# Performance work log

Hardware: AMD Instinct MI355X
Metric: run time of the kernel (lower is better)

Reference implementation:

```python
import jax, jax.numpy as jnp
import numpy as np


def setup_inputs() -> dict:
    key = jax.random.key(0)
    k0, k1, k2, k3 = jax.random.split(key, 4)
    N, C, H, W, s = 2, 16, 96, 96, 2
    x = jax.random.normal(k0, (N, C, H, W), dtype=jnp.float32)
    pos_mat = jax.random.uniform(k1, (1, H * s * W * s, 3), dtype=jnp.float32)
    mask = jnp.ones((1, 1, H * s, W * s), dtype=bool)
    w1 = jax.random.normal(k2, (3, 256), dtype=jnp.float32) * 0.1
    b1 = jnp.zeros((256,), dtype=jnp.float32)
    w2 = jax.random.normal(k3, (256, 9 * C * C), dtype=jnp.float32) * 0.02
    b2 = jnp.zeros((9 * C * C,), dtype=jnp.float32)
    return {"x": x, "pos_mat": pos_mat, "mask": mask, "w1": w1, "b1": b1,
            "w2": w2, "b2": b2, "r": 2, "hr0": H * s, "hr1": W * s}


def _unfold3x3(x):
    # torch F.unfold(x, kernel_size=3, padding=1) -> [N, C*9, H*W],
    # channel ordering: c slowest, then (kh, kw).
    N, C, H, W = x.shape
    xp = jnp.pad(x, ((0, 0), (0, 0), (1, 1), (1, 1)))
    patches = jnp.stack([xp[:, :, i:i + H, j:j + W]
                         for i in range(3) for j in range(3)], axis=2)  # [N,C,9,H,W]
    return patches.reshape(N, C * 9, H * W)


def reference(x, pos_mat, mask, w1, b1, w2, b2, r, hr0, hr1):
    s = int(np.ceil(r))  # scale_int
    N, C, H, W = x.shape

    # Pos2Weight hypernetwork: Linear(3,256) -> LeakyReLU(0.2) -> Linear(256, 9*C*C)
    p = pos_mat.reshape(-1, 3)                       # [H*s*W*s, 3]
    h = p @ w1 + b1
    h = jnp.where(h >= 0, h, 0.2 * h)
    lw = h @ w2 + b2                                 # [H*s*W*s, 9*C*C]

    # local_weight -> (s^2, H*W, 9C, C)
    lw = lw.reshape(H, s, W, s, 9 * C, C).transpose(1, 3, 0, 2, 4, 5)
    lw = lw.reshape(s * s, H * W, 9 * C, C)

    # repeat_x tiles x s^2 times along batch; all copies are identical, so the
    # unfold of up_x equals the unfold of x broadcast over the s^2 axis.
    cols = _unfold3x3(x).transpose(0, 2, 1)          # [N, H*W, 9C]

    # per-pixel batched matmul: (N,1,HW,1,9C) @ (s^2,HW,9C,C)
    out = jnp.einsum('npk,qpkc->nqpc', cols, lw)     # [N, s^2, H*W, C]

    # (N,s,s,H,W,C) -> (N,C,H,s,W,s) -> (N,C,sH,sW)
    out = out.reshape(N, s, s, H, W, C).transpose(0, 5, 3, 1, 4, 2)
    out = out.reshape(N, C, s * H, s * W)

    # masked_select with an all-True broadcast mask followed by reshape to
    # (N, C, hr0, hr1); with integer scale, hr == (sH, sW) and this is identity.
    re_sr = jnp.reshape(out, (N, C, hr0, hr1))
    return re_sr
```

## Files before the change

### kernel.cpp

```cpp
#include <hip/hip_runtime.h>
#include <stdint.h>

typedef __attribute__((ext_vector_type(8))) short          s16x8;
typedef __attribute__((ext_vector_type(8))) unsigned short u16x8;
typedef __attribute__((ext_vector_type(4))) float          f32x4;

#define KPAD  160
#define MROWS 18432
#define HWPIX 9216
#define ASTR  168
#define OSTR  68

static __device__ __forceinline__ unsigned short f2bf(float f) {
  unsigned int u = __float_as_uint(f);
  u += 0x7fffu + ((u >> 16) & 1u);
  return (unsigned short)(u >> 16);
}

__global__ __launch_bounds__(256)
void ml_prep(const float* __restrict__ x, const float* __restrict__ w2,
             const float* __restrict__ b2,
             unsigned short* __restrict__ Aimg, unsigned short* __restrict__ Btimg)
{
  int idx = blockIdx.x * 256 + threadIdx.x;
  if (idx < 368640) {
    int r = idx / 20, kb = idx - (idx / 20) * 20;
    int p = r >> 1, n2 = r & 1;
    int hh = p / 96, ww = p - hh * 96;
    u16x8 v;
#pragma unroll
    for (int t = 0; t < 8; t++) {
      int k = kb * 8 + t;
      float xv = 0.f;
      if (k < 144) {
        int cc = k / 9, kidx = k - cc * 9;
        int ih = hh + kidx / 3 - 1, iw = ww + (kidx % 3) - 1;
        if (ih >= 0 && ih < 96 && iw >= 0 && iw < 96)
          xv = x[((n2 * 16 + cc) * 96 + ih) * 96 + iw];
      }
      v[t] = f2bf(xv);
    }
    *(u16x8*)(Aimg + r * KPAD + kb * 8) = v;
    return;
  }
  idx -= 368640;
  if (idx < 87040) {
    int n = idx / 20, kb = idx - (idx / 20) * 20;
    u16x8 v;
    if (n < 4096) {
      int j = n >> 4, c = n & 15;
#pragma unroll
      for (int t = 0; t < 8; t++) {
        int k = kb * 8 + t;
        v[t] = (k < 144) ? f2bf(w2[j * 2304 + k * 16 + c]) : (unsigned short)0;
      }
    } else {
      int m = n - 4096;
      int jl = m >> 4, c = m & 15;
#pragma unroll
      for (int t = 0; t < 8; t++) {
        int k = kb * 8 + t;
        v[t] = (jl == 0 && k < 144) ? f2bf(b2[k * 16 + c]) : (unsigned short)0;
      }
    }
    *(u16x8*)(Btimg + n * KPAD + kb * 8) = v;
  }
}

struct SmemT {
  unsigned short A[64 * ASTR];
  float hbuf[2][32 * OSTR];
};

static __device__ __forceinline__ void load_bfrag(s16x8* br,
    const unsigned short* __restrict__ Bt, int n0, int ks, int lane, int wid)
{
#pragma unroll
  for (int ni = 0; ni < 4; ni++) {
    int col = wid * 64 + ni * 16 + (lane & 15);
    br[ni] = *(const s16x8*)(Bt + (n0 + col) * KPAD + ks * 32 + (lane >> 4) * 8);
  }
}

__global__ __launch_bounds__(256, 2)
void ml_main(const unsigned short* __restrict__ Aimg,
             const unsigned short* __restrict__ Btimg,
             const float* __restrict__ pos, const float* __restrict__ w1,
             const float* __restrict__ b1,
             float* __restrict__ out)
{
  __shared__ SmemT sm;
  const int tid  = threadIdx.x;
  const int lane = tid & 63;
  const int wid  = tid >> 6;
  const int bx   = blockIdx.x;
  const int m0   = bx * 64;
  const int p0   = bx * 32;

  u16x8 av[5];
  int arow[5], akb[5];
#pragma unroll
  for (int i = 0; i < 5; i++) {
    int id = i * 256 + tid;
    arow[i] = id / 20; akb[i] = id - (id / 20) * 20;
    av[i] = *(const u16x8*)(Aimg + (m0 + arow[i]) * KPAD + akb[i] * 8);
  }

  float pv[4][3];
  {
    int p = p0 + (tid >> 3);
    int hh = p / 96, ww = p - hh * 96;
#pragma unroll
    for (int q = 0; q < 4; q++) {
      int m = hh * 384 + (q >> 1) * 192 + ww * 2 + (q & 1);
      pv[q][0] = pos[m * 3 + 0];
      pv[q][1] = pos[m * 3 + 1];
      pv[q][2] = pos[m * 3 + 2];
    }
  }

#pragma unroll
  for (int i = 0; i < 5; i++)
    *(u16x8*)(sm.A + arow[i] * ASTR + akb[i] * 8) = av[i];

  s16x8 br0[4], br1[4];
  load_bfrag(br0, Btimg, 0, 0, lane, wid);

  f32x4 oa[4][4];
#pragma unroll
  for (int mi = 0; mi < 4; mi++)
#pragma unroll
    for (int reg = 0; reg < 4; reg++) {
      f32x4 z = {0.f, 0.f, 0.f, 0.f};
      oa[mi][reg] = z;
    }

  __syncthreads();

  auto jblock = [&](int jb, s16x8 (&bx0)[4], s16x8 (&bx1)[4]) {
    {
      float* hb = sm.hbuf[jb & 1];
      int p_h = tid >> 3, sub = tid & 7;
#pragma unroll
      for (int t = 0; t < 2; t++) {
        int jl = sub + t * 8;
        f32x4 hv;
        if (jb < 16) {
          int j = jb * 16 + jl;
          float wa = w1[j], wb = w1[256 + j], wc = w1[512 + j], bb = b1[j];
#pragma unroll
          for (int q = 0; q < 4; q++) {
            float h = pv[q][0] * wa + pv[q][1] * wb + pv[q][2] * wc + bb;
            hv[q] = (h >= 0.f) ? h : 0.2f * h;
          }
        } else {
          float v = (jl == 0) ? 1.f : 0.f;
          hv[0] = v; hv[1] = v; hv[2] = v; hv[3] = v;
        }
        *(f32x4*)&hb[p_h * OSTR + jl * 4] = hv;
      }
    }
    __syncthreads();

    f32x4 acc[4][4];
#pragma unroll
    for (int mi = 0; mi < 4; mi++)
#pragma unroll
      for (int ni = 0; ni < 4; ni++) {
        f32x4 z = {0.f, 0.f, 0.f, 0.f};
        acc[mi][ni] = z;
      }

#pragma unroll
    for (int ks = 0; ks < 5; ks++) {
      s16x8 (&bcur)[4]  = (ks & 1) ? bx1 : bx0;
      s16x8 (&bnext)[4] = (ks & 1) ? bx0 : bx1;
      if (!(jb == 16 && ks == 4)) {
        int njb = (ks < 4) ? jb : jb + 1;
        int nks = (ks < 4) ? ks + 1 : 0;
        load_bfrag(bnext, Btimg, njb * 256, nks, lane, wid);
      }
      s16x8 af[4];
#pragma unroll
      for (int mi = 0; mi < 4; mi++) {
        int row = mi * 16 + (lane & 15);
        af[mi] = *(const s16x8*)(sm.A + row * ASTR + ks * 32 + (lane >> 4) * 8);
      }
#pragma unroll
      for (int mi = 0; mi < 4; mi++)
#pragma unroll
        for (int ni = 0; ni < 4; ni++)
          acc[mi][ni] = __builtin_amdgcn_mfma_f32_16x16x32_bf16(af[mi], bcur[ni], acc[mi][ni], 0, 0, 0);
    }

    {
      const float* hb = sm.hbuf[jb & 1];
#pragma unroll
      for (int mi = 0; mi < 4; mi++) {
        int pb = mi * 8 + (lane >> 4) * 2;
#pragma unroll
        for (int ni = 0; ni < 4; ni++) {
          int jl = wid * 4 + ni;
          const float* hp = &hb[pb * OSTR + jl * 4];
          f32x4 h0 = *(const f32x4*)hp;
          f32x4 h1 = *(const f32x4*)(hp + OSTR);
          f32x4 a = acc[mi][ni];
          oa[mi][0] += h0 * a[0];
          oa[mi][1] += h0 * a[1];
          oa[mi][2] += h1 * a[2];
          oa[mi][3] += h1 * a[3];
        }
      }
    }
  };

#pragma unroll 1
  for (int jb2 = 0; jb2 < 8; jb2++) {
    jblock(2 * jb2,     br0, br1);
    jblock(2 * jb2 + 1, br1, br0);
  }
  jblock(16, br0, br1);

  float* outr = (float*)sm.A;
  __syncthreads();
  if (wid == 0) {
#pragma unroll
    for (int mi = 0; mi < 4; mi++)
#pragma unroll
      for (int reg = 0; reg < 4; reg++) {
        int row = mi * 16 + (lane >> 4) * 4 + reg;
        *(f32x4*)&outr[row * OSTR + (lane & 15) * 4] = oa[mi][reg];
      }
  }
  __syncthreads();
#pragma unroll 1
  for (int r = 1; r < 4; r++) {
    if (wid == r) {
#pragma unroll
      for (int mi = 0; mi < 4; mi++)
#pragma unroll
        for (int reg = 0; reg < 4; reg++) {
          int row = mi * 16 + (lane >> 4) * 4 + reg;
          f32x4* dst = (f32x4*)&outr[row * OSTR + (lane & 15) * 4];
          *dst += oa[mi][reg];
        }
    }
    __syncthreads();
  }

  const int hh0 = bx / 3;
  const int ww0 = (bx - hh0 * 3) * 32;
#pragma unroll 1
  for (int i = 0; i < 16; i++) {
    int flat = i * 256 + tid;
    int xl = flat & 63;
    int si = (flat >> 6) & 1;
    int c  = (flat >> 7) & 15;
    int n2 = flat >> 11;
    int pl = xl >> 1, sj = xl & 1;
    int q = si * 2 + sj;
    int row = pl * 2 + n2;
    float v = outr[row * OSTR + c * 4 + q];
    out[((n2 * 16 + c) * 192 + hh0 * 2 + si) * 192 + ww0 * 2 + xl] = v;
  }
}

extern "C" void kernel_launch(void* const* d_in, const int* in_sizes, int n_in,
                              void* d_out, int out_size, void* d_ws, size_t ws_size,
                              hipStream_t stream) {
  const float* x   = (const float*)d_in[0];
  const float* pos = (const float*)d_in[1];
  const float* w1  = (const float*)d_in[3];
  const float* b1  = (const float*)d_in[4];
  const float* w2  = (const float*)d_in[5];
  const float* b2  = (const float*)d_in[6];
  float* out = (float*)d_out;

  unsigned short* Aimg  = (unsigned short*)d_ws;
  unsigned short* Btimg = Aimg + MROWS * KPAD;

  ml_prep<<<1780, 256, 0, stream>>>(x, w2, b2, Aimg, Btimg);
  ml_main<<<288, 256, 0, stream>>>(Aimg, Btimg, pos, w1, b1, out);
}
```

Before: 80.86 us.

## Split hidden dimension across two blocks with atomic reduction and pre-fragmented operands

The main kernel's grid doubles by splitting the 17 hidden-unit blocks between two y-blocks. Each y-block accumulates a partial output that is combined into a zeroed output buffer with atomicAdd, and the prep kernel now also zeroes that buffer. A and B operands are prewritten in MFMA fragment order so loads become contiguous lane-strided vectors and the padded LDS stride is dropped. This is meant to raise occupancy and parallelism on a 288-block grid, at the cost of atomic traffic, redundant A loads and hypernetwork setup per y-block, and nondeterministic float summation order.

```diff
diff --git a/kernel.cpp b/kernel.cpp
--- a/kernel.cpp
+++ b/kernel.cpp
@@ -5,11 +5,9 @@
 typedef __attribute__((ext_vector_type(8))) unsigned short u16x8;
 typedef __attribute__((ext_vector_type(4))) float          f32x4;
 
-#define KPAD  160
-#define MROWS 18432
 #define HWPIX 9216
-#define ASTR  168
 #define OSTR  68
+#define ABLK  10240
 
 static __device__ __forceinline__ unsigned short f2bf(float f) {
   unsigned int u = __float_as_uint(f);
@@ -20,17 +18,21 @@
 __global__ __launch_bounds__(256)
 void ml_prep(const float* __restrict__ x, const float* __restrict__ w2,
              const float* __restrict__ b2,
-             unsigned short* __restrict__ Aimg, unsigned short* __restrict__ Btimg)
+             unsigned short* __restrict__ Afrag, unsigned short* __restrict__ Bfrag,
+             float* __restrict__ out)
 {
   int idx = blockIdx.x * 256 + threadIdx.x;
   if (idx < 368640) {
-    int r = idx / 20, kb = idx - (idx / 20) * 20;
-    int p = r >> 1, n2 = r & 1;
+    int bx = idx / 1280, r = idx - bx * 1280;
+    int ks = r >> 8, mi = (r >> 6) & 3, lane = r & 63;
+    int row = bx * 64 + mi * 16 + (lane & 15);
+    int p = row >> 1, n2 = row & 1;
     int hh = p / 96, ww = p - hh * 96;
+    int k0 = ks * 32 + (lane >> 4) * 8;
     u16x8 v;
 #pragma unroll
     for (int t = 0; t < 8; t++) {
-      int k = kb * 8 + t;
+      int k = k0 + t;
       float xv = 0.f;
       if (k < 144) {
         int cc = k / 9, kidx = k - cc * 9;
@@ -40,51 +42,56 @@
       }
       v[t] = f2bf(xv);
     }
-    *(u16x8*)(Aimg + r * KPAD + kb * 8) = v;
+    *(u16x8*)(Afrag + (size_t)idx * 8) = v;
     return;
   }
   idx -= 368640;
   if (idx < 87040) {
-    int n = idx / 20, kb = idx - (idx / 20) * 20;
+    int lane = idx & 63;
+    int q  = idx >> 6;
+    int ni = q & 3;
+    int q2 = q >> 2;
+    int ks = q2 % 5;
+    int q3 = q2 / 5;
+    int wid = q3 & 3;
+    int jb  = q3 >> 2;
+    int col = jb * 256 + wid * 64 + ni * 16 + (lane & 15);
+    int k0 = ks * 32 + (lane >> 4) * 8;
     u16x8 v;
-    if (n < 4096) {
-      int j = n >> 4, c = n & 15;
+    if (col < 4096) {
+      int j = col >> 4, c = col & 15;
 #pragma unroll
       for (int t = 0; t < 8; t++) {
-        int k = kb * 8 + t;
+        int k = k0 + t;
         v[t] = (k < 144) ? f2bf(w2[j * 2304 + k * 16 + c]) : (unsigned short)0;
       }
     } else {
-      int m = n - 4096;
+      int m = col - 4096;
       int jl = m >> 4, c = m & 15;
 #pragma unroll
       for (int t = 0; t < 8; t++) {
-        int k = kb * 8 + t;
+        int k = k0 + t;
         v[t] = (jl == 0 && k < 144) ? f2bf(b2[k * 16 + c]) : (unsigned short)0;
       }
     }
-    *(u16x8*)(Btimg + n * KPAD + kb * 8) = v;
+    *(u16x8*)(Bfrag + (size_t)idx * 8) = v;
+    return;
+  }
+  idx -= 87040;
+  if (idx < 294912) {
+    f32x4 z = {0.f, 0.f, 0.f, 0.f};
+    ((f32x4*)out)[idx] = z;
   }
 }
 
 struct SmemT {
-  unsigned short A[64 * ASTR];
+  unsigned short A[ABLK];
   float hbuf[2][32 * OSTR];
 };
 
-static __device__ __forceinline__ void load_bfrag(s16x8* br,
-    const unsigned short* __restrict__ Bt, int n0, int ks, int lane, int wid)
-{
-#pragma unroll
-  for (int ni = 0; ni < 4; ni++) {
-    int col = wid * 64 + ni * 16 + (lane & 15);
-    br[ni] = *(const s16x8*)(Bt + (n0 + col) * KPAD + ks * 32 + (lane >> 4) * 8);
-  }
-}
-
 __global__ __launch_bounds__(256, 2)
-void ml_main(const unsigned short* __restrict__ Aimg,
-             const unsigned short* __restrict__ Btimg,
+void ml_main(const unsigned short* __restrict__ Afrag,
+             const unsigned short* __restrict__ Bfrag,
              const float* __restrict__ pos, const float* __restrict__ w1,
              const float* __restrict__ b1,
              float* __restrict__ out)
@@ -94,17 +101,16 @@
   const int lane = tid & 63;
   const int wid  = tid >> 6;
   const int bx   = blockIdx.x;
-  const int m0   = bx * 64;
+  const int jy   = blockIdx.y;
   const int p0   = bx * 32;
-
+  const int jb0     = jy ? 8 : 0;
+  const int jb_last = jy ? 16 : 7;
+
+  const unsigned short* Ablk = Afrag + (size_t)bx * ABLK;
   u16x8 av[5];
-  int arow[5], akb[5];
-#pragma unroll
-  for (int i = 0; i < 5; i++) {
-    int id = i * 256 + tid;
-    arow[i] = id / 20; akb[i] = id - (id / 20) * 20;
-    av[i] = *(const u16x8*)(Aimg + (m0 + arow[i]) * KPAD + akb[i] * 8);
-  }
+#pragma unroll
+  for (int i = 0; i < 5; i++)
+    av[i] = *(const u16x8*)(Ablk + (i * 256 + tid) * 8);
 
   float pv[4][3];
   {
@@ -121,10 +127,15 @@
 
 #pragma unroll
   for (int i = 0; i < 5; i++)
-    *(u16x8*)(sm.A + arow[i] * ASTR + akb[i] * 8) = av[i];
+    *(u16x8*)(sm.A + (i * 256 + tid) * 8) = av[i];
 
   s16x8 br0[4], br1[4];
-  load_bfrag(br0, Btimg, 0, 0, lane, wid);
+  {
+    const unsigned short* bb = Bfrag + ((size_t)((jb0 * 4 + wid) * 5) * 4) * 512 + lane * 8;
+#pragma unroll
+    for (int ni = 0; ni < 4; ni++)
+      br0[ni] = *(const s16x8*)(bb + ni * 512);
+  }
 
   f32x4 oa[4][4];
 #pragma unroll
@@ -175,17 +186,19 @@
     for (int ks = 0; ks < 5; ks++) {
       s16x8 (&bcur)[4]  = (ks & 1) ? bx1 : bx0;
       s16x8 (&bnext)[4] = (ks & 1) ? bx0 : bx1;
-      if (!(jb == 16 && ks == 4)) {
+      if (!(jb == jb_last && ks == 4)) {
         int njb = (ks < 4) ? jb : jb + 1;
         int nks = (ks < 4) ? ks + 1 : 0;
-        load_bfrag(bnext, Btimg, njb * 256, nks, lane, wid);
+        const unsigned short* bb = Bfrag
+            + ((size_t)(((njb * 4 + wid) * 5 + nks) * 4)) * 512 + lane * 8;
+#pragma unroll
+        for (int ni = 0; ni < 4; ni++)
+          bnext[ni] = *(const s16x8*)(bb + ni * 512);
       }
       s16x8 af[4];
 #pragma unroll
-      for (int mi = 0; mi < 4; mi++) {
-        int row = mi * 16 + (lane & 15);
-        af[mi] = *(const s16x8*)(sm.A + row * ASTR + ks * 32 + (lane >> 4) * 8);
-      }
+      for (int mi = 0; mi < 4; mi++)
+        af[mi] = *(const s16x8*)(sm.A + (ks * 4 + mi) * 512 + lane * 8);
 #pragma unroll
       for (int mi = 0; mi < 4; mi++)
 #pragma unroll
@@ -215,11 +228,11 @@
   };
 
 #pragma unroll 1
-  for (int jb2 = 0; jb2 < 8; jb2++) {
-    jblock(2 * jb2,     br0, br1);
-    jblock(2 * jb2 + 1, br1, br0);
-  }
-  jblock(16, br0, br1);
+  for (int jb2 = 0; jb2 < 4; jb2++) {
+    jblock(jb0 + 2 * jb2,     br0, br1);
+    jblock(jb0 + 2 * jb2 + 1, br1, br0);
+  }
+  if (jy) jblock(16, br0, br1);
 
   float* outr = (float*)sm.A;
   __syncthreads();
@@ -261,7 +274,7 @@
     int q = si * 2 + sj;
     int row = pl * 2 + n2;
     float v = outr[row * OSTR + c * 4 + q];
-    out[((n2 * 16 + c) * 192 + hh0 * 2 + si) * 192 + ww0 * 2 + xl] = v;
+    atomicAdd(&out[((n2 * 16 + c) * 192 + hh0 * 2 + si) * 192 + ww0 * 2 + xl], v);
   }
 }
 
@@ -276,9 +289,9 @@
   const float* b2  = (const float*)d_in[6];
   float* out = (float*)d_out;
 
-  unsigned short* Aimg  = (unsigned short*)d_ws;
-  unsigned short* Btimg = Aimg + MROWS * KPAD;
-
-  ml_prep<<<1780, 256, 0, stream>>>(x, w2, b2, Aimg, Btimg);
-  ml_main<<<288, 256, 0, stream>>>(Aimg, Btimg, pos, w1, b1, out);
-}
+  unsigned short* Afrag = (unsigned short*)d_ws;
+  unsigned short* Bfrag = Afrag + (size_t)288 * ABLK;
+
+  ml_prep<<<2932, 256, 0, stream>>>(x, w2, b2, Afrag, Bfrag, out);
+  ml_main<<<dim3(288, 2), 256, 0, stream>>>(Afrag, Bfrag, pos, w1, b1, out);
+}
```

Result: slower. 280.8 us (+247.3%).

## Split j-blocks across two wave groups and pre-swizzle A into MFMA fragment layout

Applied to the files above, without the earlier changes.

The main kernel now runs 512 threads per block: two groups of four waves each handle alternating j-blocks of the hypernetwork contraction. The two partial outputs are reduced through shared memory at the end. The prep kernel writes A directly in MFMA fragment order, so the shared-memory A loads become contiguous per lane and the padded stride goes away. The aim is more waves per CU to hide B-fragment global-load latency, with only 288 blocks on the device. The cost is extra hbuf shared memory, an extra reduction buffer, and more register pressure under launch_bounds(512,2).

```diff
diff --git a/kernel.cpp b/kernel.cpp
--- a/kernel.cpp
+++ b/kernel.cpp
@@ -6,10 +6,9 @@
 typedef __attribute__((ext_vector_type(4))) float          f32x4;
 
 #define KPAD  160
-#define MROWS 18432
 #define HWPIX 9216
-#define ASTR  168
 #define OSTR  68
+#define ABLK  10240
 
 static __device__ __forceinline__ unsigned short f2bf(float f) {
   unsigned int u = __float_as_uint(f);
@@ -20,17 +19,20 @@
 __global__ __launch_bounds__(256)
 void ml_prep(const float* __restrict__ x, const float* __restrict__ w2,
              const float* __restrict__ b2,
-             unsigned short* __restrict__ Aimg, unsigned short* __restrict__ Btimg)
+             unsigned short* __restrict__ Afrag, unsigned short* __restrict__ Btimg)
 {
   int idx = blockIdx.x * 256 + threadIdx.x;
   if (idx < 368640) {
-    int r = idx / 20, kb = idx - (idx / 20) * 20;
-    int p = r >> 1, n2 = r & 1;
+    int bx = idx / 1280, r = idx - bx * 1280;
+    int ks = r >> 8, mi = (r >> 6) & 3, lane = r & 63;
+    int row = bx * 64 + mi * 16 + (lane & 15);
+    int p = row >> 1, n2 = row & 1;
     int hh = p / 96, ww = p - hh * 96;
+    int k0 = ks * 32 + (lane >> 4) * 8;
     u16x8 v;
 #pragma unroll
     for (int t = 0; t < 8; t++) {
-      int k = kb * 8 + t;
+      int k = k0 + t;
       float xv = 0.f;
       if (k < 144) {
         int cc = k / 9, kidx = k - cc * 9;
@@ -40,7 +42,7 @@
       }
       v[t] = f2bf(xv);
     }
-    *(u16x8*)(Aimg + r * KPAD + kb * 8) = v;
+    *(u16x8*)(Afrag + (size_t)idx * 8) = v;
     return;
   }
   idx -= 368640;
@@ -68,22 +70,12 @@
 }
 
 struct SmemT {
-  unsigned short A[64 * ASTR];
-  float hbuf[2][32 * OSTR];
+  unsigned short A[ABLK];
+  float hbuf[2][2][32 * OSTR];
 };
 
-static __device__ __forceinline__ void load_bfrag(s16x8* br,
-    const unsigned short* __restrict__ Bt, int n0, int ks, int lane, int wid)
-{
-#pragma unroll
-  for (int ni = 0; ni < 4; ni++) {
-    int col = wid * 64 + ni * 16 + (lane & 15);
-    br[ni] = *(const s16x8*)(Bt + (n0 + col) * KPAD + ks * 32 + (lane >> 4) * 8);
-  }
-}
-
-__global__ __launch_bounds__(256, 2)
-void ml_main(const unsigned short* __restrict__ Aimg,
+__global__ __launch_bounds__(512, 2)
+void ml_main(const unsigned short* __restrict__ Afrag,
              const unsigned short* __restrict__ Btimg,
              const float* __restrict__ pos, const float* __restrict__ w1,
              const float* __restrict__ b1,
@@ -93,22 +85,22 @@
   const int tid  = threadIdx.x;
   const int lane = tid & 63;
   const int wid  = tid >> 6;
+  const int wni  = wid & 3;
+  const int wjb  = wid >> 2;
   const int bx   = blockIdx.x;
-  const int m0   = bx * 64;
   const int p0   = bx * 32;
 
-  u16x8 av[5];
-  int arow[5], akb[5];
-#pragma unroll
-  for (int i = 0; i < 5; i++) {
-    int id = i * 256 + tid;
-    arow[i] = id / 20; akb[i] = id - (id / 20) * 20;
-    av[i] = *(const u16x8*)(Aimg + (m0 + arow[i]) * KPAD + akb[i] * 8);
+  const unsigned short* Ablk = Afrag + (size_t)bx * ABLK;
+  u16x8 av[3];
+#pragma unroll
+  for (int i = 0; i < 3; i++) {
+    int aid = i * 512 + tid;
+    if (aid < 1280) av[i] = *(const u16x8*)(Ablk + aid * 8);
   }
 
   float pv[4][3];
   {
-    int p = p0 + (tid >> 3);
+    int p = p0 + (tid >> 4);
     int hh = p / 96, ww = p - hh * 96;
 #pragma unroll
     for (int q = 0; q < 4; q++) {
@@ -120,11 +112,17 @@
   }
 
 #pragma unroll
-  for (int i = 0; i < 5; i++)
-    *(u16x8*)(sm.A + arow[i] * ASTR + akb[i] * 8) = av[i];
+  for (int i = 0; i < 3; i++) {
+    int aid = i * 512 + tid;
+    if (aid < 1280) *(u16x8*)(sm.A + aid * 8) = av[i];
+  }
 
   s16x8 br0[4], br1[4];
-  load_bfrag(br0, Btimg, 0, 0, lane, wid);
+#pragma unroll
+  for (int ni = 0; ni < 4; ni++) {
+    int col = wjb * 256 + wni * 64 + ni * 16 + (lane & 15);
+    br0[ni] = *(const s16x8*)(Btimg + col * KPAD + (lane >> 4) * 8);
+  }
 
   f32x4 oa[4][4];
 #pragma unroll
@@ -137,70 +135,74 @@
 
   __syncthreads();
 
-  auto jblock = [&](int jb, s16x8 (&bx0)[4], s16x8 (&bx1)[4]) {
+  auto step = [&](int s, s16x8 (&bx0)[4], s16x8 (&bx1)[4]) {
     {
-      float* hb = sm.hbuf[jb & 1];
-      int p_h = tid >> 3, sub = tid & 7;
-#pragma unroll
-      for (int t = 0; t < 2; t++) {
-        int jl = sub + t * 8;
-        f32x4 hv;
-        if (jb < 16) {
-          int j = jb * 16 + jl;
-          float wa = w1[j], wb = w1[256 + j], wc = w1[512 + j], bb = b1[j];
-#pragma unroll
-          for (int q = 0; q < 4; q++) {
-            float h = pv[q][0] * wa + pv[q][1] * wb + pv[q][2] * wc + bb;
-            hv[q] = (h >= 0.f) ? h : 0.2f * h;
+      int p_h = tid >> 4, jl = tid & 15;
+#pragma unroll
+      for (int wj = 0; wj < 2; wj++) {
+        int jb = 2 * s + wj;
+        if (jb <= 16) {
+          f32x4 hv;
+          if (jb < 16) {
+            int j = jb * 16 + jl;
+            float wa = w1[j], wb = w1[256 + j], wc = w1[512 + j], bb = b1[j];
+#pragma unroll
+            for (int q = 0; q < 4; q++) {
+              float h = pv[q][0] * wa + pv[q][1] * wb + pv[q][2] * wc + bb;
+              hv[q] = (h >= 0.f) ? h : 0.2f * h;
+            }
+          } else {
+            float v = (jl == 0) ? 1.f : 0.f;
+            hv[0] = v; hv[1] = v; hv[2] = v; hv[3] = v;
           }
-        } else {
-          float v = (jl == 0) ? 1.f : 0.f;
-          hv[0] = v; hv[1] = v; hv[2] = v; hv[3] = v;
-        }
-        *(f32x4*)&hb[p_h * OSTR + jl * 4] = hv;
+          *(f32x4*)&sm.hbuf[s & 1][wj][p_h * OSTR + jl * 4] = hv;
+        }
       }
     }
     __syncthreads();
 
-    f32x4 acc[4][4];
-#pragma unroll
-    for (int mi = 0; mi < 4; mi++)
-#pragma unroll
-      for (int ni = 0; ni < 4; ni++) {
-        f32x4 z = {0.f, 0.f, 0.f, 0.f};
-        acc[mi][ni] = z;
-      }
-
-#pragma unroll
-    for (int ks = 0; ks < 5; ks++) {
-      s16x8 (&bcur)[4]  = (ks & 1) ? bx1 : bx0;
-      s16x8 (&bnext)[4] = (ks & 1) ? bx0 : bx1;
-      if (!(jb == 16 && ks == 4)) {
-        int njb = (ks < 4) ? jb : jb + 1;
-        int nks = (ks < 4) ? ks + 1 : 0;
-        load_bfrag(bnext, Btimg, njb * 256, nks, lane, wid);
-      }
-      s16x8 af[4];
-#pragma unroll
-      for (int mi = 0; mi < 4; mi++) {
-        int row = mi * 16 + (lane & 15);
-        af[mi] = *(const s16x8*)(sm.A + row * ASTR + ks * 32 + (lane >> 4) * 8);
-      }
+    const int jb_w = 2 * s + wjb;
+    if (jb_w <= 16) {
+      f32x4 acc[4][4];
 #pragma unroll
       for (int mi = 0; mi < 4; mi++)
 #pragma unroll
-        for (int ni = 0; ni < 4; ni++)
-          acc[mi][ni] = __builtin_amdgcn_mfma_f32_16x16x32_bf16(af[mi], bcur[ni], acc[mi][ni], 0, 0, 0);
-    }
-
-    {
-      const float* hb = sm.hbuf[jb & 1];
+        for (int ni = 0; ni < 4; ni++) {
+          f32x4 z = {0.f, 0.f, 0.f, 0.f};
+          acc[mi][ni] = z;
+        }
+
+#pragma unroll
+      for (int ks = 0; ks < 5; ks++) {
+        s16x8 (&bcur)[4]  = (ks & 1) ? bx1 : bx0;
+        s16x8 (&bnext)[4] = (ks & 1) ? bx0 : bx1;
+        if (ks < 4 || jb_w + 2 <= 16) {
+          int njb = (ks < 4) ? jb_w : jb_w + 2;
+          int nks = (ks < 4) ? ks + 1 : 0;
+#pragma unroll
+          for (int ni = 0; ni < 4; ni++) {
+            int col = njb * 256 + wni * 64 + ni * 16 + (lane & 15);
+            bnext[ni] = *(const s16x8*)(Btimg + col * KPAD + nks * 32 + (lane >> 4) * 8);
+          }
+        }
+        s16x8 af[4];
+#pragma unroll
+        for (int mi = 0; mi < 4; mi++)
+          af[mi] = *(const s16x8*)(sm.A + (ks * 4 + mi) * 512 + lane * 8);
+#pragma unroll
+        for (int mi = 0; mi < 4; mi++)
+#pragma unroll
+          for (int ni = 0; ni < 4; ni++)
+            acc[mi][ni] = __builtin_amdgcn_mfma_f32_16x16x32_bf16(af[mi], bcur[ni], acc[mi][ni], 0, 0, 0);
+      }
+
+      const float* hb = &sm.hbuf[s & 1][wjb][0];
 #pragma unroll
       for (int mi = 0; mi < 4; mi++) {
         int pb = mi * 8 + (lane >> 4) * 2;
 #pragma unroll
         for (int ni = 0; ni < 4; ni++) {
-          int jl = wid * 4 + ni;
+          int jl = wni * 4 + ni;
           const float* hp = &hb[pb * OSTR + jl * 4];
           f32x4 h0 = *(const f32x4*)hp;
           f32x4 h1 = *(const f32x4*)(hp + OSTR);
@@ -215,34 +217,37 @@
   };
 
 #pragma unroll 1
-  for (int jb2 = 0; jb2 < 8; jb2++) {
-    jblock(2 * jb2,     br0, br1);
-    jblock(2 * jb2 + 1, br1, br0);
-  }
-  jblock(16, br0, br1);
-
-  float* outr = (float*)sm.A;
+  for (int s2 = 0; s2 < 4; s2++) {
+    step(2 * s2,     br0, br1);
+    step(2 * s2 + 1, br1, br0);
+  }
+  step(8, br0, br1);
+
+  float* outr  = (float*)sm.A;
+  float* outr2 = (float*)&sm.hbuf[0][0][0];
   __syncthreads();
-  if (wid == 0) {
+  if (wid == 0 || wid == 4) {
+    float* dst = (wid == 0) ? outr : outr2;
 #pragma unroll
     for (int mi = 0; mi < 4; mi++)
 #pragma unroll
       for (int reg = 0; reg < 4; reg++) {
         int row = mi * 16 + (lane >> 4) * 4 + reg;
-        *(f32x4*)&outr[row * OSTR + (lane & 15) * 4] = oa[mi][reg];
+        *(f32x4*)&dst[row * OSTR + (lane & 15) * 4] = oa[mi][reg];
       }
   }
   __syncthreads();
 #pragma unroll 1
   for (int r = 1; r < 4; r++) {
-    if (wid == r) {
+    if (wid == r || wid == r + 4) {
+      float* dst = (wid == r) ? outr : outr2;
 #pragma unroll
       for (int mi = 0; mi < 4; mi++)
 #pragma unroll
         for (int reg = 0; reg < 4; reg++) {
           int row = mi * 16 + (lane >> 4) * 4 + reg;
-          f32x4* dst = (f32x4*)&outr[row * OSTR + (lane & 15) * 4];
-          *dst += oa[mi][reg];
+          f32x4* d = (f32x4*)&dst[row * OSTR + (lane & 15) * 4];
+          *d += oa[mi][reg];
         }
     }
     __syncthreads();
@@ -251,8 +256,8 @@
   const int hh0 = bx / 3;
   const int ww0 = (bx - hh0 * 3) * 32;
 #pragma unroll 1
-  for (int i = 0; i < 16; i++) {
-    int flat = i * 256 + tid;
+  for (int i = 0; i < 8; i++) {
+    int flat = i * 512 + tid;
     int xl = flat & 63;
     int si = (flat >> 6) & 1;
     int c  = (flat >> 7) & 15;
@@ -260,7 +265,8 @@
     int pl = xl >> 1, sj = xl & 1;
     int q = si * 2 + sj;
     int row = pl * 2 + n2;
-    float v = outr[row * OSTR + c * 4 + q];
+    int idx = row * OSTR + c * 4 + q;
+    float v = outr[idx] + outr2[idx];
     out[((n2 * 16 + c) * 192 + hh0 * 2 + si) * 192 + ww0 * 2 + xl] = v;
   }
 }
@@ -276,9 +282,9 @@
   const float* b2  = (const float*)d_in[6];
   float* out = (float*)d_out;
 
-  unsigned short* Aimg  = (unsigned short*)d_ws;
-  unsigned short* Btimg = Aimg + MROWS * KPAD;
-
-  ml_prep<<<1780, 256, 0, stream>>>(x, w2, b2, Aimg, Btimg);
-  ml_main<<<288, 256, 0, stream>>>(Aimg, Btimg, pos, w1, b1, out);
-}
+  unsigned short* Afrag = (unsigned short*)d_ws;
+  unsigned short* Btimg = Afrag + (size_t)288 * ABLK;
+
+  ml_prep<<<1780, 256, 0, stream>>>(x, w2, b2, Afrag, Btimg);
+  ml_main<<<288, 512, 0, stream>>>(Afrag, Btimg, pos, w1, b1, out);
+}
```

Result: slower. 92.65 us (+14.6%).
